# Performance work log

Hardware: AMD Instinct MI355X
Metric: run time of the kernel (lower is better)

The kernel has to match this reference:

```python
import jax, jax.numpy as jnp
import numpy as np

EMBED_DIM = 512
NUM_HEADS = 8
HEAD_DIM = EMBED_DIM // NUM_HEADS
B, N = 2, 4096


def setup_inputs() -> dict:
    key = jax.random.key(0)
    ks = jax.random.split(key, 5)
    x = jax.random.normal(ks[0], (B, N, EMBED_DIM), dtype=jnp.float32)
    # causal mask: 1 where attention is allowed (j <= i), 0 elsewhere
    mask = jnp.tril(jnp.ones((N, N), dtype=jnp.int32))[None, None]  # [1,1,N,N]
    s_in = 1.0 / np.sqrt(EMBED_DIM)
    qkv_w = jax.random.uniform(ks[1], (3 * EMBED_DIM, EMBED_DIM), jnp.float32, -s_in, s_in)
    qkv_b = jax.random.uniform(ks[2], (3 * EMBED_DIM,), jnp.float32, -s_in, s_in)
    out_w = jax.random.uniform(ks[3], (EMBED_DIM, EMBED_DIM), jnp.float32, -s_in, s_in)
    out_b = jax.random.uniform(ks[4], (EMBED_DIM,), jnp.float32, -s_in, s_in)
    return {"x": x, "mask": mask, "qkv_w": qkv_w, "qkv_b": qkv_b,
            "out_w": out_w, "out_b": out_b}


def reference(x, mask, qkv_w, qkv_b, out_w, out_b):
    Bc, Nc, C = x.shape
    H, D = NUM_HEADS, HEAD_DIM
    scale = D ** (-0.5)
    qkv = x @ qkv_w.T + qkv_b                      # [B,N,3C]
    qkv = qkv.reshape(Bc, Nc, 3, H, D)
    q = jnp.transpose(qkv[:, :, 0], (0, 2, 1, 3))  # [B,H,N,D]
    k = jnp.transpose(qkv[:, :, 1], (0, 2, 1, 3))
    v = jnp.transpose(qkv[:, :, 2], (0, 2, 1, 3))
    scores = jnp.einsum('bhqd,bhkd->bhqk', q, k) * scale
    scores = jnp.where(mask == 0, -jnp.inf, scores)
    attn = jax.nn.softmax(scores, axis=-1)         # dropout p=0 (eval)
    out = jnp.einsum('bhqk,bhkd->bhqd', attn, v)   # [B,H,N,D]
    out = jnp.transpose(out, (0, 2, 1, 3)).reshape(Bc, Nc, C)
    return out @ out_w.T + out_b
```

## Files before the change

kernel.cpp:

```cpp
#include <hip/hip_runtime.h>
#include <hip/hip_bf16.h>
#include <cstdint>
#include <cstddef>

#define EMBED 512
#define NHEADS 8
#define HDIM 64
#define BATCH 2
#define SEQ 4096
#define TOKENS (BATCH*SEQ)
#define QSCALE 0.1803368801f

typedef __attribute__((ext_vector_type(8))) short short8;
typedef __attribute__((ext_vector_type(4))) float floatx4;

__device__ __forceinline__ unsigned short f2bf(float f){
  unsigned int u = __float_as_uint(f);
  u += 0x7fff + ((u >> 16) & 1);
  return (unsigned short)(u >> 16);
}

__device__ __forceinline__ unsigned int pkbf(float a, float b){
  unsigned int ra = __float_as_uint(a) + 0x8000u;
  unsigned int rb = __float_as_uint(b) + 0x8000u;
  return __builtin_amdgcn_perm(rb, ra, 0x07060302u);
}

__device__ __forceinline__ void gl2lds16(const unsigned short* g, unsigned short* l){
  __builtin_amdgcn_global_load_lds(
      (const __attribute__((address_space(1))) unsigned int*)g,
      (__attribute__((address_space(3))) unsigned int*)l, 16, 0, 0);
}

#define XN4  (TOKENS*EMBED/4)
#define W1N4 (3*EMBED*EMBED/4)
#define W2N4 (EMBED*EMBED/4)
__global__ void cvt_all(const float* __restrict__ x, const float* __restrict__ w1,
                        const float* __restrict__ w2, unsigned short* __restrict__ out){
  int i = blockIdx.x*blockDim.x + threadIdx.x;
  const float* s; int j;
  if (i < XN4){ s = x; j = i; }
  else if (i < XN4+W1N4){ s = w1; j = i - XN4; }
  else { s = w2; j = i - (XN4+W1N4); }
  float4 v = reinterpret_cast<const float4*>(s)[j];
  ushort4 o; o.x=f2bf(v.x); o.y=f2bf(v.y); o.z=f2bf(v.z); o.w=f2bf(v.w);
  reinterpret_cast<ushort4*>(out)[i] = o;
}

template<int MODE>
__global__ __launch_bounds__(256) void gemm_bt(
    const unsigned short* __restrict__ A,
    const unsigned short* __restrict__ Bw,
    const float* __restrict__ bias,
    unsigned short* __restrict__ Qb,
    unsigned short* __restrict__ Kb,
    unsigned short* __restrict__ Vb,
    float* __restrict__ Cout)
{
  const int K = EMBED;
  __shared__ unsigned short Al[128*64];
  __shared__ unsigned short Bl[128*64];
  const int tm = blockIdx.x * 128;
  const int tn = blockIdx.y * 128;
  const int tid = threadIdx.x;
  const int w = tid >> 6, lane = tid & 63;
  const int m16 = lane & 15, q4 = lane >> 4;
  const int wm = w & 1, wn = w >> 1;
  const bool transp = (MODE == 1) || (tn < 2*EMBED);

  floatx4 acc[4][4];
  #pragma unroll
  for (int i=0;i<4;i++)
    #pragma unroll
    for (int j=0;j<4;j++) acc[i][j] = (floatx4){0.f,0.f,0.f,0.f};

  const int srow = tid >> 3, p8 = tid & 7, c8 = p8 ^ (srow & 7);

  for (int k0 = 0; k0 < K; k0 += 64){
    __syncthreads();
    #pragma unroll
    for (int cal=0; cal<4; cal++){
      gl2lds16(A  + (size_t)(tm + cal*32 + srow)*K + k0 + c8*8, Al + cal*2048 + tid*8);
      gl2lds16(Bw + (size_t)(tn + cal*32 + srow)*K + k0 + c8*8, Bl + cal*2048 + tid*8);
    }
    __syncthreads();
    short8 af[4][2], bfv[4][2];
    #pragma unroll
    for (int i=0;i<4;i++)
      #pragma unroll
      for (int s=0;s<2;s++)
        af[i][s] = *reinterpret_cast<const short8*>(Al + (wm*64 + i*16 + m16)*64 + (((s*4+q4) ^ (m16&7))*8));
    #pragma unroll
    for (int j=0;j<4;j++)
      #pragma unroll
      for (int s=0;s<2;s++)
        bfv[j][s] = *reinterpret_cast<const short8*>(Bl + (wn*64 + j*16 + m16)*64 + (((s*4+q4) ^ (m16&7))*8));
    #pragma unroll
    for (int i=0;i<4;i++)
      #pragma unroll
      for (int j=0;j<4;j++)
        #pragma unroll
        for (int s=0;s<2;s++){
          if (transp)
            acc[i][j] = __builtin_amdgcn_mfma_f32_16x16x32_bf16(bfv[j][s], af[i][s], acc[i][j], 0,0,0);
          else
            acc[i][j] = __builtin_amdgcn_mfma_f32_16x16x32_bf16(af[i][s], bfv[j][s], acc[i][j], 0,0,0);
        }
  }

  if (MODE == 1){
    #pragma unroll
    for (int j=0;j<4;j++){
      const int col0 = tn + wn*64 + j*16 + q4*4;
      const float4 bv = *reinterpret_cast<const float4*>(bias + col0);
      #pragma unroll
      for (int i=0;i<4;i++){
        const int row = tm + wm*64 + i*16 + m16;
        float4 o;
        o.x = acc[i][j][0] + bv.x; o.y = acc[i][j][1] + bv.y;
        o.z = acc[i][j][2] + bv.z; o.w = acc[i][j][3] + bv.w;
        *reinterpret_cast<float4*>(Cout + (size_t)row*EMBED + col0) = o;
      }
    }
    return;
  }

  if (transp){
    #pragma unroll
    for (int j=0;j<4;j++){
      const int col0 = tn + wn*64 + j*16 + q4*4;
      const int which = col0 >> 9, h = (col0 >> 6) & 7, d0 = col0 & 63;
      const float4 bv = *reinterpret_cast<const float4*>(bias + col0);
      #pragma unroll
      for (int i=0;i<4;i++){
        const int row = tm + wm*64 + i*16 + m16;
        const int b = row >> 12, n = row & (SEQ-1);
        float v0 = acc[i][j][0] + bv.x, v1 = acc[i][j][1] + bv.y;
        float v2 = acc[i][j][2] + bv.z, v3 = acc[i][j][3] + bv.w;
        unsigned short* dst;
        if (which == 0){
          v0 *= QSCALE; v1 *= QSCALE; v2 *= QSCALE; v3 *= QSCALE;
          dst = Qb + ((size_t)(b*NHEADS + h)*SEQ + n)*HDIM + d0;
        } else {
          dst = Kb + ((size_t)(b*NHEADS + h)*SEQ + n)*HDIM + d0;
        }
        uint2 pk; pk.x = pkbf(v0, v1); pk.y = pkbf(v2, v3);
        *reinterpret_cast<uint2*>(dst) = pk;
      }
    }
  } else {
    #pragma unroll
    for (int j=0;j<4;j++){
      const int col = tn + wn*64 + j*16 + m16;
      const float bv = bias[col];
      const int h = (col >> 6) & 7, d = col & 63;
      #pragma unroll
      for (int i=0;i<4;i++){
        const int row0 = tm + wm*64 + i*16 + q4*4;
        const int b = row0 >> 12, n0 = row0 & (SEQ-1);
        uint2 pk;
        pk.x = pkbf(acc[i][j][0] + bv, acc[i][j][1] + bv);
        pk.y = pkbf(acc[i][j][2] + bv, acc[i][j][3] + bv);
        *reinterpret_cast<uint2*>(Vb + ((size_t)(b*NHEADS + h)*HDIM + d)*SEQ + n0) = pk;
      }
    }
  }
}

__global__ __launch_bounds__(512) void flash_attn(
  const unsigned short* __restrict__ Qb,
  const unsigned short* __restrict__ Kb,
  const unsigned short* __restrict__ Vb,
  unsigned short* __restrict__ Ob)
{
  __shared__ unsigned short KVl[2][2*64*64];
  __shared__ unsigned short Pl[8][16*72];

  const int blk = blockIdx.x;
  const int qt = (blk < 256) ? (31 - (blk >> 4)) : ((blk >> 4) - 16);
  const int bh = blk & 15;
  const int qbase = qt * 128;
  const unsigned short* Qh = Qb + (size_t)bh*SEQ*HDIM;
  const unsigned short* Kh = Kb + (size_t)bh*SEQ*HDIM;
  const unsigned short* Vh = Vb + (size_t)bh*HDIM*SEQ;

  const int tid = threadIdx.x, w = tid>>6, lane = tid&63;
  const int m16 = lane & 15, q4 = lane >> 4;
  const int srow = tid >> 3, p8 = tid & 7, c8 = p8 ^ (srow & 7);
  const int x7 = m16 & 7;

  short8 ones;
  #pragma unroll
  for (int i=0;i<8;i++) ones[i] = (short)0x3F80;

  const int rowg0 = qbase + w*16;
  short8 qf0, qf1;
  {
    const unsigned short* qp = Qh + (size_t)(rowg0 + m16)*HDIM + q4*8;
    qf0 = *reinterpret_cast<const short8*>(qp);
    qf1 = *reinterpret_cast<const short8*>(qp + 32);
  }

  floatx4 oacc[4];
  floatx4 lacc = (floatx4){0.f,0.f,0.f,0.f};
  #pragma unroll
  for (int t=0;t<4;t++) oacc[t] = (floatx4){0.f,0.f,0.f,0.f};

  const int jtmax = 2*qt + 1;

  auto stage = [&](int jt, int buf){
    gl2lds16(Kh + (size_t)(jt*64 + srow)*HDIM + c8*8, &KVl[buf][tid*8]);
    gl2lds16(Vh + (size_t)srow*SEQ + jt*64 + c8*8,    &KVl[buf][64*64 + tid*8]);
  };

  stage(0, 0);
  for (int jt = 0; jt <= jtmax; jt++){
    const int cur = jt & 1;
    const int jbase = jt*64;
    __syncthreads();
    if (jt < jtmax) stage(jt+1, cur^1);
    if (jbase > rowg0 + 15) continue;
    const unsigned short* Kl = &KVl[cur][0];
    const unsigned short* Vl = &KVl[cur][64*64];

    floatx4 s[4];
    #pragma unroll
    for (int t=0;t<4;t++){
      floatx4 a = (floatx4){0.f,0.f,0.f,0.f};
      short8 kf0 = *reinterpret_cast<const short8*>(Kl + (t*16 + m16)*64 + ((q4     ^ x7)*8));
      short8 kf1 = *reinterpret_cast<const short8*>(Kl + (t*16 + m16)*64 + (((q4+4) ^ x7)*8));
      a = __builtin_amdgcn_mfma_f32_16x16x32_bf16(kf0, qf0, a, 0,0,0);
      a = __builtin_amdgcn_mfma_f32_16x16x32_bf16(kf1, qf1, a, 0,0,0);
      s[t] = a;
    }

    const bool diag = (jbase + 63 > rowg0);
    #pragma unroll
    for (int t=0;t<4;t++){
      #pragma unroll
      for (int r=0;r<4;r++){
        float p = exp2f(s[t][r]);
        if (diag){
          const int key = jbase + t*16 + q4*4 + r;
          if (key > rowg0 + m16) p = 0.f;
        }
        s[t][r] = p;
      }
      uint2 pk;
      pk.x = pkbf(s[t][0], s[t][1]);
      pk.y = pkbf(s[t][2], s[t][3]);
      *reinterpret_cast<uint2*>(&Pl[w][m16*72 + t*16 + q4*4]) = pk;
    }

    short8 pf0 = *reinterpret_cast<const short8*>(&Pl[w][m16*72 + q4*8]);
    short8 pf1 = *reinterpret_cast<const short8*>(&Pl[w][m16*72 + 32 + q4*8]);

    lacc = __builtin_amdgcn_mfma_f32_16x16x32_bf16(pf0, ones, lacc, 0,0,0);
    lacc = __builtin_amdgcn_mfma_f32_16x16x32_bf16(pf1, ones, lacc, 0,0,0);

    #pragma unroll
    for (int t=0;t<4;t++){
      short8 vf0 = *reinterpret_cast<const short8*>(Vl + (t*16 + m16)*64 + ((q4     ^ x7)*8));
      short8 vf1 = *reinterpret_cast<const short8*>(Vl + (t*16 + m16)*64 + (((q4+4) ^ x7)*8));
      oacc[t] = __builtin_amdgcn_mfma_f32_16x16x32_bf16(pf0, vf0, oacc[t], 0,0,0);
      oacc[t] = __builtin_amdgcn_mfma_f32_16x16x32_bf16(pf1, vf1, oacc[t], 0,0,0);
    }
  }

  const int b = bh >> 3, h = bh & 7;
  #pragma unroll
  for (int r=0;r<4;r++){
    const float inv = 1.0f / lacc[r];
    const int n = rowg0 + q4*4 + r;
    const size_t base = ((size_t)(b*SEQ + n))*EMBED + h*HDIM;
    #pragma unroll
    for (int t=0;t<4;t++)
      Ob[base + t*16 + m16] = f2bf(oacc[t][r] * inv);
  }
}

extern "C" void kernel_launch(void* const* d_in, const int* in_sizes, int n_in,
                              void* d_out, int out_size, void* d_ws, size_t ws_size,
                              hipStream_t stream){
  const float* x      = (const float*)d_in[0];
  const float* qkv_w  = (const float*)d_in[2];
  const float* qkv_b  = (const float*)d_in[3];
  const float* out_w  = (const float*)d_in[4];
  const float* out_b  = (const float*)d_in[5];
  float* out = (float*)d_out;

  unsigned short* ws = (unsigned short*)d_ws;
  unsigned short* xb  = ws;
  unsigned short* qwb = xb  + (size_t)TOKENS*EMBED;
  unsigned short* owb = qwb + (size_t)3*EMBED*EMBED;
  unsigned short* Qb  = owb + (size_t)EMBED*EMBED;
  unsigned short* Kb  = Qb  + (size_t)BATCH*NHEADS*SEQ*HDIM;
  unsigned short* Vb  = Kb  + (size_t)BATCH*NHEADS*SEQ*HDIM;
  unsigned short* Ob  = Vb  + (size_t)BATCH*NHEADS*SEQ*HDIM;

  cvt_all<<<dim3((XN4+W1N4+W2N4)/256), 256, 0, stream>>>(x, qkv_w, out_w, xb);
  gemm_bt<0><<<dim3(TOKENS/128, 3*EMBED/128), 256, 0, stream>>>(xb, qwb, qkv_b, Qb, Kb, Vb, nullptr);
  flash_attn<<<dim3(SEQ/128*16), 512, 0, stream>>>(Qb, Kb, Vb, Ob);
  gemm_bt<1><<<dim3(TOKENS/128, EMBED/128), 256, 0, stream>>>(Ob, owb, out_b, nullptr, nullptr, nullptr, out);
}
```

Before: 246.4 us.

## Switch flash attention to 32x32 MFMA tiles with four waves per block

The attention kernel moves from 16x16x32 to 32x32x16 bf16 MFMA. Each wave now owns 32 query rows instead of 16, and the block shrinks from 8 to 4 waves, with the staging loads doubled per thread to still fill the 64-key K/V tile. The larger tiles raise data reuse per LDS read and cut the number of MFMA issues, and the masking branch is hoisted out of the exp loop. In exchange, accumulator register pressure grows and there are fewer waves per block to hide latency.

```diff
diff --git a/kernel.cpp b/kernel.cpp
--- a/kernel.cpp
+++ b/kernel.cpp
@@ -13,6 +13,7 @@
 
 typedef __attribute__((ext_vector_type(8))) short short8;
 typedef __attribute__((ext_vector_type(4))) float floatx4;
+typedef __attribute__((ext_vector_type(16))) float floatx16;
 
 __device__ __forceinline__ unsigned short f2bf(float f){
   unsigned int u = __float_as_uint(f);
@@ -167,14 +168,14 @@
   }
 }
 
-__global__ __launch_bounds__(512) void flash_attn(
+__global__ __launch_bounds__(256) void flash_attn(
   const unsigned short* __restrict__ Qb,
   const unsigned short* __restrict__ Kb,
   const unsigned short* __restrict__ Vb,
   unsigned short* __restrict__ Ob)
 {
   __shared__ unsigned short KVl[2][2*64*64];
-  __shared__ unsigned short Pl[8][16*72];
+  __shared__ unsigned short Pl[4][32*72];
 
   const int blk = blockIdx.x;
   const int qt = (blk < 256) ? (31 - (blk >> 4)) : ((blk >> 4) - 16);
@@ -185,32 +186,37 @@
   const unsigned short* Vh = Vb + (size_t)bh*HDIM*SEQ;
 
   const int tid = threadIdx.x, w = tid>>6, lane = tid&63;
-  const int m16 = lane & 15, q4 = lane >> 4;
+  const int l31 = lane & 31, hi = lane >> 5;
+  const int x7 = l31 & 7;
   const int srow = tid >> 3, p8 = tid & 7, c8 = p8 ^ (srow & 7);
-  const int x7 = m16 & 7;
 
   short8 ones;
   #pragma unroll
   for (int i=0;i<8;i++) ones[i] = (short)0x3F80;
 
-  const int rowg0 = qbase + w*16;
-  short8 qf0, qf1;
+  const int rowg0 = qbase + w*32;
+  short8 qf[4];
   {
-    const unsigned short* qp = Qh + (size_t)(rowg0 + m16)*HDIM + q4*8;
-    qf0 = *reinterpret_cast<const short8*>(qp);
-    qf1 = *reinterpret_cast<const short8*>(qp + 32);
-  }
-
-  floatx4 oacc[4];
-  floatx4 lacc = (floatx4){0.f,0.f,0.f,0.f};
+    const unsigned short* qp = Qh + (size_t)(rowg0 + l31)*HDIM + hi*8;
+    #pragma unroll
+    for (int s=0;s<4;s++)
+      qf[s] = *reinterpret_cast<const short8*>(qp + 16*s);
+  }
+
+  floatx16 oacc[2];
+  floatx16 lacc;
   #pragma unroll
-  for (int t=0;t<4;t++) oacc[t] = (floatx4){0.f,0.f,0.f,0.f};
+  for (int i=0;i<16;i++){ oacc[0][i]=0.f; oacc[1][i]=0.f; lacc[i]=0.f; }
 
   const int jtmax = 2*qt + 1;
 
   auto stage = [&](int jt, int buf){
-    gl2lds16(Kh + (size_t)(jt*64 + srow)*HDIM + c8*8, &KVl[buf][tid*8]);
-    gl2lds16(Vh + (size_t)srow*SEQ + jt*64 + c8*8,    &KVl[buf][64*64 + tid*8]);
+    const unsigned short* Kp = Kh + (size_t)(jt*64 + srow)*HDIM + c8*8;
+    gl2lds16(Kp,           &KVl[buf][tid*8]);
+    gl2lds16(Kp + 32*HDIM, &KVl[buf][32*64 + tid*8]);
+    const unsigned short* Vp = Vh + (size_t)srow*SEQ + jt*64 + c8*8;
+    gl2lds16(Vp,           &KVl[buf][64*64 + tid*8]);
+    gl2lds16(Vp + 32*SEQ,  &KVl[buf][64*64 + 32*64 + tid*8]);
   };
 
   stage(0, 0);
@@ -219,63 +225,83 @@
     const int jbase = jt*64;
     __syncthreads();
     if (jt < jtmax) stage(jt+1, cur^1);
-    if (jbase > rowg0 + 15) continue;
+    if (jbase > rowg0 + 31) continue;
     const unsigned short* Kl = &KVl[cur][0];
     const unsigned short* Vl = &KVl[cur][64*64];
 
-    floatx4 s[4];
-    #pragma unroll
-    for (int t=0;t<4;t++){
-      floatx4 a = (floatx4){0.f,0.f,0.f,0.f};
-      short8 kf0 = *reinterpret_cast<const short8*>(Kl + (t*16 + m16)*64 + ((q4     ^ x7)*8));
-      short8 kf1 = *reinterpret_cast<const short8*>(Kl + (t*16 + m16)*64 + (((q4+4) ^ x7)*8));
-      a = __builtin_amdgcn_mfma_f32_16x16x32_bf16(kf0, qf0, a, 0,0,0);
-      a = __builtin_amdgcn_mfma_f32_16x16x32_bf16(kf1, qf1, a, 0,0,0);
-      s[t] = a;
+    floatx16 sacc[2];
+    #pragma unroll
+    for (int t=0;t<2;t++){
+      floatx16 a;
+      #pragma unroll
+      for (int i=0;i<16;i++) a[i] = 0.f;
+      #pragma unroll
+      for (int s=0;s<4;s++){
+        short8 kf = *reinterpret_cast<const short8*>(
+            Kl + (t*32 + l31)*64 + (((2*s + hi) ^ x7)*8));
+        a = __builtin_amdgcn_mfma_f32_32x32x16_bf16(kf, qf[s], a, 0,0,0);
+      }
+      sacc[t] = a;
     }
 
     const bool diag = (jbase + 63 > rowg0);
-    #pragma unroll
-    for (int t=0;t<4;t++){
-      #pragma unroll
-      for (int r=0;r<4;r++){
-        float p = exp2f(s[t][r]);
-        if (diag){
-          const int key = jbase + t*16 + q4*4 + r;
-          if (key > rowg0 + m16) p = 0.f;
+    if (diag){
+      #pragma unroll
+      for (int t=0;t<2;t++)
+        #pragma unroll
+        for (int reg=0; reg<16; reg++){
+          const int key = jbase + t*32 + (reg&3) + 8*(reg>>2) + 4*hi;
+          float p = exp2f(sacc[t][reg]);
+          if (key > rowg0 + l31) p = 0.f;
+          sacc[t][reg] = p;
         }
-        s[t][r] = p;
-      }
-      uint2 pk;
-      pk.x = pkbf(s[t][0], s[t][1]);
-      pk.y = pkbf(s[t][2], s[t][3]);
-      *reinterpret_cast<uint2*>(&Pl[w][m16*72 + t*16 + q4*4]) = pk;
-    }
-
-    short8 pf0 = *reinterpret_cast<const short8*>(&Pl[w][m16*72 + q4*8]);
-    short8 pf1 = *reinterpret_cast<const short8*>(&Pl[w][m16*72 + 32 + q4*8]);
-
-    lacc = __builtin_amdgcn_mfma_f32_16x16x32_bf16(pf0, ones, lacc, 0,0,0);
-    lacc = __builtin_amdgcn_mfma_f32_16x16x32_bf16(pf1, ones, lacc, 0,0,0);
-
-    #pragma unroll
-    for (int t=0;t<4;t++){
-      short8 vf0 = *reinterpret_cast<const short8*>(Vl + (t*16 + m16)*64 + ((q4     ^ x7)*8));
-      short8 vf1 = *reinterpret_cast<const short8*>(Vl + (t*16 + m16)*64 + (((q4+4) ^ x7)*8));
-      oacc[t] = __builtin_amdgcn_mfma_f32_16x16x32_bf16(pf0, vf0, oacc[t], 0,0,0);
-      oacc[t] = __builtin_amdgcn_mfma_f32_16x16x32_bf16(pf1, vf1, oacc[t], 0,0,0);
+    } else {
+      #pragma unroll
+      for (int t=0;t<2;t++)
+        #pragma unroll
+        for (int reg=0; reg<16; reg++)
+          sacc[t][reg] = exp2f(sacc[t][reg]);
+    }
+
+    #pragma unroll
+    for (int t=0;t<2;t++)
+      #pragma unroll
+      for (int g=0; g<4; g++){
+        uint2 pk;
+        pk.x = pkbf(sacc[t][4*g+0], sacc[t][4*g+1]);
+        pk.y = pkbf(sacc[t][4*g+2], sacc[t][4*g+3]);
+        *reinterpret_cast<uint2*>(&Pl[w][l31*72 + t*32 + 8*g + 4*hi]) = pk;
+      }
+
+    short8 pf[4];
+    #pragma unroll
+    for (int s=0;s<4;s++)
+      pf[s] = *reinterpret_cast<const short8*>(&Pl[w][l31*72 + hi*8 + 16*s]);
+
+    #pragma unroll
+    for (int s=0;s<4;s++)
+      lacc = __builtin_amdgcn_mfma_f32_32x32x16_bf16(pf[s], ones, lacc, 0,0,0);
+    #pragma unroll
+    for (int dt=0; dt<2; dt++){
+      floatx16 a = oacc[dt];
+      #pragma unroll
+      for (int s=0;s<4;s++){
+        short8 vf = *reinterpret_cast<const short8*>(
+            Vl + (dt*32 + l31)*64 + (((2*s + hi) ^ x7)*8));
+        a = __builtin_amdgcn_mfma_f32_32x32x16_bf16(pf[s], vf, a, 0,0,0);
+      }
+      oacc[dt] = a;
     }
   }
 
   const int b = bh >> 3, h = bh & 7;
   #pragma unroll
-  for (int r=0;r<4;r++){
-    const float inv = 1.0f / lacc[r];
-    const int n = rowg0 + q4*4 + r;
+  for (int reg=0; reg<16; reg++){
+    const float inv = 1.0f / lacc[reg];
+    const int n = rowg0 + (reg&3) + 8*(reg>>2) + 4*hi;
     const size_t base = ((size_t)(b*SEQ + n))*EMBED + h*HDIM;
-    #pragma unroll
-    for (int t=0;t<4;t++)
-      Ob[base + t*16 + m16] = f2bf(oacc[t][r] * inv);
+    Ob[base + l31]      = f2bf(oacc[0][reg] * inv);
+    Ob[base + 32 + l31] = f2bf(oacc[1][reg] * inv);
   }
 }
 
@@ -300,6 +326,6 @@
 
   cvt_all<<<dim3((XN4+W1N4+W2N4)/256), 256, 0, stream>>>(x, qkv_w, out_w, xb);
   gemm_bt<0><<<dim3(TOKENS/128, 3*EMBED/128), 256, 0, stream>>>(xb, qwb, qkv_b, Qb, Kb, Vb, nullptr);
-  flash_attn<<<dim3(SEQ/128*16), 512, 0, stream>>>(Qb, Kb, Vb, Ob);
+  flash_attn<<<dim3(SEQ/128*16), 256, 0, stream>>>(Qb, Kb, Vb, Ob);
   gemm_bt<1><<<dim3(TOKENS/128, EMBED/128), 256, 0, stream>>>(Ob, owb, out_b, nullptr, nullptr, nullptr, out);
 }
```

New measurement: 260.6 us. +5.8%, slower.

## Shrink attention query tile to 64 rows and keep P in registers

Applied to the files above, without the earlier changes.

The flash attention kernel now processes 64 query rows per block with 256 threads instead of 128 rows with 512 threads, doubling the grid and adjusting K/V staging so each thread issues two loads per tensor. The P probabilities are packed straight into MFMA operand registers, with V fragments read in a permuted order to match. This removes the per-warp LDS round trip and its buffer. It also splits the mask and no-mask exp paths and uses the hardware exp2 builtin. Smaller tiles raise occupancy and improve causal load balance, but each K/V tile is reused by fewer query rows, so total K/V traffic rises.

```diff
diff --git a/kernel.cpp b/kernel.cpp
--- a/kernel.cpp
+++ b/kernel.cpp
@@ -13,6 +13,18 @@
 
 typedef __attribute__((ext_vector_type(8))) short short8;
 typedef __attribute__((ext_vector_type(4))) float floatx4;
+
+#if defined(__has_builtin)
+# if __has_builtin(__builtin_amdgcn_exp2f)
+#  define EXP2F(x) __builtin_amdgcn_exp2f(x)
+# else
+#  define EXP2F(x) exp2f(x)
+# endif
+#else
+# define EXP2F(x) exp2f(x)
+#endif
+
+union U8 { uint4 u; short8 s; };
 
 __device__ __forceinline__ unsigned short f2bf(float f){
   unsigned int u = __float_as_uint(f);
@@ -167,19 +179,18 @@
   }
 }
 
-__global__ __launch_bounds__(512) void flash_attn(
+__global__ __launch_bounds__(256, 4) void flash_attn(
   const unsigned short* __restrict__ Qb,
   const unsigned short* __restrict__ Kb,
   const unsigned short* __restrict__ Vb,
   unsigned short* __restrict__ Ob)
 {
   __shared__ unsigned short KVl[2][2*64*64];
-  __shared__ unsigned short Pl[8][16*72];
 
   const int blk = blockIdx.x;
-  const int qt = (blk < 256) ? (31 - (blk >> 4)) : ((blk >> 4) - 16);
+  const int qt = (blk < 512) ? (63 - (blk >> 4)) : ((blk >> 4) - 32);
   const int bh = blk & 15;
-  const int qbase = qt * 128;
+  const int qbase = qt * 64;
   const unsigned short* Qh = Qb + (size_t)bh*SEQ*HDIM;
   const unsigned short* Kh = Kb + (size_t)bh*SEQ*HDIM;
   const unsigned short* Vh = Vb + (size_t)bh*HDIM*SEQ;
@@ -188,6 +199,7 @@
   const int m16 = lane & 15, q4 = lane >> 4;
   const int srow = tid >> 3, p8 = tid & 7, c8 = p8 ^ (srow & 7);
   const int x7 = m16 & 7;
+  const int q4l = q4 & 1, q4h = q4 >> 1;
 
   short8 ones;
   #pragma unroll
@@ -206,19 +218,27 @@
   #pragma unroll
   for (int t=0;t<4;t++) oacc[t] = (floatx4){0.f,0.f,0.f,0.f};
 
-  const int jtmax = 2*qt + 1;
-
-  auto stage = [&](int jt, int buf){
-    gl2lds16(Kh + (size_t)(jt*64 + srow)*HDIM + c8*8, &KVl[buf][tid*8]);
-    gl2lds16(Vh + (size_t)srow*SEQ + jt*64 + c8*8,    &KVl[buf][64*64 + tid*8]);
-  };
-
-  stage(0, 0);
-  for (int jt = 0; jt <= jtmax; jt++){
+  const unsigned short* ks = Kh + (size_t)srow*HDIM + c8*8;
+  const unsigned short* vs = Vh + (size_t)srow*SEQ + c8*8;
+
+  gl2lds16(ks,            &KVl[0][tid*8]);
+  gl2lds16(ks + 32*HDIM,  &KVl[0][32*64 + tid*8]);
+  gl2lds16(vs,            &KVl[0][64*64 + tid*8]);
+  gl2lds16(vs + 32*SEQ,   &KVl[0][64*64 + 32*64 + tid*8]);
+  ks += 64*HDIM; vs += 64;
+
+  for (int jt = 0; jt <= qt; jt++){
     const int cur = jt & 1;
     const int jbase = jt*64;
     __syncthreads();
-    if (jt < jtmax) stage(jt+1, cur^1);
+    if (jt < qt){
+      unsigned short* dst = &KVl[cur^1][0];
+      gl2lds16(ks,           dst + tid*8);
+      gl2lds16(ks + 32*HDIM, dst + 32*64 + tid*8);
+      gl2lds16(vs,           dst + 64*64 + tid*8);
+      gl2lds16(vs + 32*SEQ,  dst + 64*64 + 32*64 + tid*8);
+      ks += 64*HDIM; vs += 64;
+    }
     if (jbase > rowg0 + 15) continue;
     const unsigned short* Kl = &KVl[cur][0];
     const unsigned short* Vl = &KVl[cur][64*64];
@@ -234,36 +254,49 @@
       s[t] = a;
     }
 
-    const bool diag = (jbase + 63 > rowg0);
-    #pragma unroll
-    for (int t=0;t<4;t++){
-      #pragma unroll
-      for (int r=0;r<4;r++){
-        float p = exp2f(s[t][r]);
-        if (diag){
+    if (jbase + 63 > rowg0){
+      #pragma unroll
+      for (int t=0;t<4;t++)
+        #pragma unroll
+        for (int r=0;r<4;r++){
+          float p = EXP2F(s[t][r]);
           const int key = jbase + t*16 + q4*4 + r;
           if (key > rowg0 + m16) p = 0.f;
+          s[t][r] = p;
         }
-        s[t][r] = p;
+    } else {
+      #pragma unroll
+      for (int t=0;t<4;t++)
+        #pragma unroll
+        for (int r=0;r<4;r++)
+          s[t][r] = EXP2F(s[t][r]);
+    }
+
+    short8 pf[2];
+    #pragma unroll
+    for (int tp=0; tp<2; tp++){
+      U8 a;
+      a.u.x = pkbf(s[2*tp][0],   s[2*tp][1]);
+      a.u.y = pkbf(s[2*tp][2],   s[2*tp][3]);
+      a.u.z = pkbf(s[2*tp+1][0], s[2*tp+1][1]);
+      a.u.w = pkbf(s[2*tp+1][2], s[2*tp+1][3]);
+      pf[tp] = a.s;
+    }
+
+    lacc = __builtin_amdgcn_mfma_f32_16x16x32_bf16(pf[0], ones, lacc, 0,0,0);
+    lacc = __builtin_amdgcn_mfma_f32_16x16x32_bf16(pf[1], ones, lacc, 0,0,0);
+
+    #pragma unroll
+    for (int dt=0; dt<4; dt++){
+      const unsigned short* vrow = Vl + (dt*16 + m16)*64;
+      #pragma unroll
+      for (int tp=0; tp<2; tp++){
+        const int g0 = 4*tp + q4h, g1 = 4*tp + 2 + q4h;
+        uint2 lo = *reinterpret_cast<const uint2*>(vrow + ((g0 ^ x7)*8) + q4l*4);
+        uint2 hi = *reinterpret_cast<const uint2*>(vrow + ((g1 ^ x7)*8) + q4l*4);
+        U8 vf; vf.u.x = lo.x; vf.u.y = lo.y; vf.u.z = hi.x; vf.u.w = hi.y;
+        oacc[dt] = __builtin_amdgcn_mfma_f32_16x16x32_bf16(pf[tp], vf.s, oacc[dt], 0,0,0);
       }
-      uint2 pk;
-      pk.x = pkbf(s[t][0], s[t][1]);
-      pk.y = pkbf(s[t][2], s[t][3]);
-      *reinterpret_cast<uint2*>(&Pl[w][m16*72 + t*16 + q4*4]) = pk;
-    }
-
-    short8 pf0 = *reinterpret_cast<const short8*>(&Pl[w][m16*72 + q4*8]);
-    short8 pf1 = *reinterpret_cast<const short8*>(&Pl[w][m16*72 + 32 + q4*8]);
-
-    lacc = __builtin_amdgcn_mfma_f32_16x16x32_bf16(pf0, ones, lacc, 0,0,0);
-    lacc = __builtin_amdgcn_mfma_f32_16x16x32_bf16(pf1, ones, lacc, 0,0,0);
-
-    #pragma unroll
-    for (int t=0;t<4;t++){
-      short8 vf0 = *reinterpret_cast<const short8*>(Vl + (t*16 + m16)*64 + ((q4     ^ x7)*8));
-      short8 vf1 = *reinterpret_cast<const short8*>(Vl + (t*16 + m16)*64 + (((q4+4) ^ x7)*8));
-      oacc[t] = __builtin_amdgcn_mfma_f32_16x16x32_bf16(pf0, vf0, oacc[t], 0,0,0);
-      oacc[t] = __builtin_amdgcn_mfma_f32_16x16x32_bf16(pf1, vf1, oacc[t], 0,0,0);
     }
   }
 
@@ -300,6 +333,6 @@
 
   cvt_all<<<dim3((XN4+W1N4+W2N4)/256), 256, 0, stream>>>(x, qkv_w, out_w, xb);
   gemm_bt<0><<<dim3(TOKENS/128, 3*EMBED/128), 256, 0, stream>>>(xb, qwb, qkv_b, Qb, Kb, Vb, nullptr);
-  flash_attn<<<dim3(SEQ/128*16), 512, 0, stream>>>(Qb, Kb, Vb, Ob);
+  flash_attn<<<dim3(SEQ/64*16), 256, 0, stream>>>(Qb, Kb, Vb, Ob);
   gemm_bt<1><<<dim3(TOKENS/128, EMBED/128), 256, 0, stream>>>(Ob, owb, out_b, nullptr, nullptr, nullptr, out);
 }
```

Result: faster. 209.5 us (-15.0%).
